# Kernel optimization log

Hardware: AMD Instinct MI355X
Metric: run time of the kernel (lower is better)

Reference implementation:

```python
import jax, jax.numpy as jnp
import numpy as np

N = 100000   # num nodes
E = 3200000  # num edges (avg degree 32)
EPS = 1e-5   # BatchNorm eps


def _gcn_norm(edge_index, edge_weight, n):
    # add self loops with weight 1 (PyG gcn_norm default fill_value=1.0)
    loops = jnp.arange(n, dtype=edge_index.dtype)
    ei = jnp.concatenate([edge_index, jnp.stack([loops, loops])], axis=1)
    ew = jnp.concatenate([edge_weight, jnp.ones((n,), edge_weight.dtype)])
    row, col = ei[0], ei[1]
    deg = jax.ops.segment_sum(ew, col, num_segments=n)
    deg_safe = jnp.where(deg > 0, deg, 1.0)
    dinv = jnp.where(deg > 0, jax.lax.rsqrt(deg_safe), 0.0)
    norm = dinv[row] * ew * dinv[col]  # [E+N]
    return row, col, norm


def _gcn_conv(x, row, col, norm, W, b, n):
    h = x @ W                                   # [N, out]
    msg = h[row] * norm[:, None]                # gather + scale, [E+N, out]
    out = jax.ops.segment_sum(msg, col, num_segments=n)  # scatter-add
    return out + b


def _bn(x, g, b, rm, rv):
    # BatchNorm1d in eval mode: running statistics
    return (x - rm) * jax.lax.rsqrt(rv + EPS) * g + b


def setup_inputs() -> dict:
    key = jax.random.key(0)
    ks = jax.random.split(key, 24)
    def p(i, shape, scale=1.0):
        return jax.random.normal(ks[i], shape, dtype=jnp.float32) * scale
    inp = {
        "x": p(0, (N, 1)),
        "edge_index": jax.random.randint(ks[1], (2, E), 0, N, dtype=jnp.int32),
        "edge_weight": jax.random.uniform(ks[2], (E,), dtype=jnp.float32),
        # GCNConv weights (glorot-ish scale) and biases
        "W1": p(3, (1, 16), 0.5), "b1": jnp.zeros((16,), jnp.float32),
        "W2": p(4, (16, 4), 0.25), "b2": jnp.zeros((4,), jnp.float32),
        "W3": p(5, (4, 1), 0.5), "b3": jnp.zeros((1,), jnp.float32),
        # BatchNorm params + running stats (running_var > 0)
        "g1": p(6, (16,), 0.1) + 1.0, "be1": p(7, (16,), 0.1),
        "rm1": p(8, (16,), 0.1), "rv1": jax.random.uniform(ks[9], (16,)) + 0.5,
        "g2": p(10, (4,), 0.1) + 1.0, "be2": p(11, (4,), 0.1),
        "rm2": p(12, (4,), 0.1), "rv2": jax.random.uniform(ks[13], (4,)) + 0.5,
        "g3": p(14, (1,), 0.1) + 1.0, "be3": p(15, (1,), 0.1),
        "rm3": p(16, (1,), 0.1), "rv3": jax.random.uniform(ks[17], (1,)) + 0.5,
        # end Linear(1, 1)
        "Wl": p(18, (1, 1)), "bl": p(19, (1,), 0.1),
    }
    return inp


def reference(x, edge_index, edge_weight,
              W1, b1, W2, b2, W3, b3,
              g1, be1, rm1, rv1,
              g2, be2, rm2, rv2,
              g3, be3, rm3, rv3,
              Wl, bl):
    row, col, norm = _gcn_norm(edge_index, edge_weight, N)
    h = _gcn_conv(x, row, col, norm, W1, b1, N)
    h = jax.nn.relu(_bn(h, g1, be1, rm1, rv1))  # dropout = identity in eval
    h = _gcn_conv(h, row, col, norm, W2, b2, N)
    h = jax.nn.relu(_bn(h, g2, be2, rm2, rv2))
    h = _gcn_conv(h, row, col, norm, W3, b3, N)
    h = _bn(h, g3, be3, rm3, rv3)
    h = h @ Wl + bl
    return jax.nn.sigmoid(h)
```

## Files before the change

### kernel.cpp

```cpp
#include <hip/hip_runtime.h>
#include <math.h>

#define NN 100000
#define NE 3200000
#define EPSBN 1e-5f

#define BSH 7
#define NB 782
#define NBLK 250
#define CHUNK 12800
#define C4 (CHUNK/4)
#define CAP 5120
#define BTA 512

#define NSB 12512
#define STCAP 4608

__global__ void k_params_zero(const float* __restrict__ W1, const float* __restrict__ b1,
                              const float* __restrict__ g1, const float* __restrict__ be1,
                              const float* __restrict__ rm1, const float* __restrict__ rv1,
                              const float* __restrict__ b2,
                              const float* __restrict__ g2, const float* __restrict__ be2,
                              const float* __restrict__ rm2, const float* __restrict__ rv2,
                              const float* __restrict__ b3,
                              const float* __restrict__ g3, const float* __restrict__ be3,
                              const float* __restrict__ rm3, const float* __restrict__ rv3,
                              const float* __restrict__ Wl, const float* __restrict__ bl,
                              float* __restrict__ P, int* __restrict__ cnt) {
    int f = threadIdx.x;
    for (int i = f; i < NB; i += 1024) cnt[i] = 0;
    if (f < 16) {
        float k = g1[f] * rsqrtf(rv1[f] + EPSBN);
        P[f]      = W1[f] * k;
        P[16 + f] = (b1[f] - rm1[f]) * k + be1[f];
    }
    if (f < 4) {
        float k = g2[f] * rsqrtf(rv2[f] + EPSBN);
        P[32 + f] = k;
        P[36 + f] = (b2[f] - rm2[f]) * k + be2[f];
    }
    if (f == 0) {
        float k = g3[0] * rsqrtf(rv3[0] + EPSBN);
        P[40] = k * Wl[0];
        P[41] = ((b3[0] - rm3[0]) * k + be3[0]) * Wl[0] + bl[0];
    }
}

__global__ void k_build(const int* __restrict__ row, const int* __restrict__ col,
                        const float* __restrict__ ew, int* __restrict__ cnt,
                        uint2* __restrict__ rec) {
    __shared__ int h[NB];
    __shared__ int base[NB];
    int blk = blockIdx.x, tid = threadIdx.x;
    for (int j = tid; j < NB; j += BTA) h[j] = 0;
    __syncthreads();
    const int4* c4 = (const int4*)(col + blk * CHUNK);
    int rk[7][4];
#pragma unroll
    for (int it = 0; it < 7; ++it) {
        int i = tid + it * BTA;
        if (i < C4) {
            int4 c = c4[i];
            rk[it][0] = atomicAdd(&h[c.x >> BSH], 1);
            rk[it][1] = atomicAdd(&h[c.y >> BSH], 1);
            rk[it][2] = atomicAdd(&h[c.z >> BSH], 1);
            rk[it][3] = atomicAdd(&h[c.w >> BSH], 1);
        }
    }
    __syncthreads();
    for (int j = tid; j < NB; j += BTA) {
        int hj = h[j];
        base[j] = hj ? atomicAdd(&cnt[j], hj) : 0;
    }
    __syncthreads();
    const int4*   r4 = (const int4*)(row + blk * CHUNK);
    const float4* w4 = (const float4*)(ew + blk * CHUNK);
#pragma unroll
    for (int it = 0; it < 7; ++it) {
        int i = tid + it * BTA;
        if (i < C4) {
            int4 c = c4[i]; int4 r = r4[i]; float4 w = w4[i];
            int b0 = c.x >> BSH, b1 = c.y >> BSH, b2 = c.z >> BSH, b3 = c.w >> BSH;
            rec[(size_t)b0 * CAP + base[b0] + rk[it][0]] =
                make_uint2((unsigned)r.x | ((unsigned)(c.x & 127) << 17), __float_as_uint(w.x));
            rec[(size_t)b1 * CAP + base[b1] + rk[it][1]] =
                make_uint2((unsigned)r.y | ((unsigned)(c.y & 127) << 17), __float_as_uint(w.y));
            rec[(size_t)b2 * CAP + base[b2] + rk[it][2]] =
                make_uint2((unsigned)r.z | ((unsigned)(c.z & 127) << 17), __float_as_uint(w.z));
            rec[(size_t)b3 * CAP + base[b3] + rk[it][3]] =
                make_uint2((unsigned)r.w | ((unsigned)(c.w & 127) << 17), __float_as_uint(w.w));
        }
    }
}

__global__ void k_subsort_deg(const int* __restrict__ cnt, uint2* __restrict__ rec,
                              int2* __restrict__ subsn, const float* __restrict__ x,
                              float* __restrict__ dinv, float* __restrict__ xd) {
    __shared__ uint2 st[STCAP];
    __shared__ int subtot[16];
    __shared__ int live[16];
    __shared__ int sstart[16];
    __shared__ int scount[16];
    int bin = blockIdx.x, tid = threadIdx.x;
    int lane = tid & 63, wv = tid >> 6;
    int n = cnt[bin];
    if (n > STCAP) n = STCAP;
    uint2* rb = rec + (size_t)bin * CAP;
    for (int i = tid; i < n; i += BTA) st[i] = rb[i];
    if (tid < 16) subtot[tid] = 0;
    __syncthreads();

    int myCnt = 0;
    for (int base = tid - lane; base < n; base += BTA) {
        int i = base + lane;
        bool v = (i < n);
        unsigned key = v ? ((st[i].x >> 20) & 15u) : 0u;
        unsigned long long bv = __ballot(v);
        unsigned long long b0 = __ballot(key & 1u);
        unsigned long long b1 = __ballot(key & 2u);
        unsigned long long b2 = __ballot(key & 4u);
        unsigned long long b3 = __ballot(key & 8u);
        if (lane < 16) {
            unsigned k = (unsigned)lane;
            unsigned long long m = bv;
            m &= (k & 1u) ? b0 : ~b0;
            m &= (k & 2u) ? b1 : ~b1;
            m &= (k & 4u) ? b2 : ~b2;
            m &= (k & 8u) ? b3 : ~b3;
            myCnt += __popcll(m);
        }
    }
    if (lane < 16 && myCnt) atomicAdd(&subtot[lane], myCnt);
    __syncthreads();

    if (tid == 0) {
        int run = 0;
        for (int k = 0; k < 16; ++k) {
            live[k] = run;
            sstart[k] = run;
            scount[k] = subtot[k];
            subsn[bin * 16 + k] = make_int2(bin * CAP + run, subtot[k]);
            run += subtot[k];
        }
    }
    __syncthreads();

    for (int base = tid - lane; base < n; base += BTA) {
        int i = base + lane;
        bool v = (i < n);
        uint2 rcd = v ? st[i] : make_uint2(0u, 0u);
        unsigned key = v ? ((rcd.x >> 20) & 15u) : 0u;
        unsigned long long bv = __ballot(v);
        unsigned long long b0 = __ballot(key & 1u);
        unsigned long long b1 = __ballot(key & 2u);
        unsigned long long b2 = __ballot(key & 4u);
        unsigned long long b3 = __ballot(key & 8u);
        int gb = 0;
        if (lane < 16) {
            unsigned k = (unsigned)lane;
            unsigned long long m = bv;
            m &= (k & 1u) ? b0 : ~b0;
            m &= (k & 2u) ? b1 : ~b1;
            m &= (k & 4u) ? b2 : ~b2;
            m &= (k & 8u) ? b3 : ~b3;
            int c = __popcll(m);
            if (c) gb = atomicAdd(&live[(int)k], c);
        }
        unsigned long long same = bv;
        same &= (key & 1u) ? b0 : ~b0;
        same &= (key & 2u) ? b1 : ~b1;
        same &= (key & 4u) ? b2 : ~b2;
        same &= (key & 8u) ? b3 : ~b3;
        unsigned long long below = (lane == 0) ? 0ull : ((~0ull) >> (64 - lane));
        int rank = __popcll(same & below);
        int mybase = __shfl(gb, (int)key);
        if (v) rb[mybase + rank] = rcd;
    }
    __syncthreads();

    for (int s = 0; s < 2; ++s) {
        int sb = (wv << 1) | s;
        int n0 = scount[sb];
        const uint2* p = rb + sstart[sb];
        float acc[8] = {0.f, 0.f, 0.f, 0.f, 0.f, 0.f, 0.f, 0.f};
        for (int i = lane; i < n0; i += 64) {
            uint2 v = p[i];
            int cl = (v.x >> 17) & 7;
            float w = __uint_as_float(v.y);
#pragma unroll
            for (int c = 0; c < 8; ++c) acc[c] += (cl == c) ? w : 0.f;
        }
#pragma unroll
        for (int c = 0; c < 8; ++c) {
            float a = acc[c];
            a += __shfl_xor(a, 1);  a += __shfl_xor(a, 2);  a += __shfl_xor(a, 4);
            a += __shfl_xor(a, 8);  a += __shfl_xor(a, 16); a += __shfl_xor(a, 32);
            acc[c] = a;
        }
        float mine = acc[0];
#pragma unroll
        for (int c = 1; c < 8; ++c) mine = (lane == c) ? acc[c] : mine;
        int colv = (bin << BSH) + (sb << 3) + lane;
        if (lane < 8 && colv < NN) {
            float d = rsqrtf(1.0f + mine);
            dinv[colv] = d;
            xd[colv] = x[colv] * d;
        }
    }
}


__global__ void k_agg1_2(const int2* __restrict__ subsn, const uint2* __restrict__ rec,
                         const float* __restrict__ dinv, const float* __restrict__ xd,
                         const float* __restrict__ P, const float* __restrict__ W2,
                         float* __restrict__ m2s) {
    __shared__ float sacc[8][8][32];
    int tid = threadIdx.x, lane = tid & 63, wv = tid >> 6;
    int b = blockIdx.x * 8 + wv;
    int2 sn = subsn[b];
    float acc[8] = {0.f, 0.f, 0.f, 0.f, 0.f, 0.f, 0.f, 0.f};
    for (int i = lane; i < sn.y; i += 64) {
        uint2 v = rec[sn.x + i];
        int cl = (v.x >> 17) & 7;
        float g = xd[v.x & 0x1FFFF] * __uint_as_float(v.y);
#pragma unroll
        for (int c = 0; c < 8; ++c) acc[c] += (cl == c) ? g : 0.f;
    }
#pragma unroll
    for (int c = 0; c < 8; ++c) acc[c] += __shfl_xor(acc[c], 32);
    if (lane < 32) {
#pragma unroll
        for (int c = 0; c < 8; ++c) sacc[wv][c][lane] = acc[c];
    }
    __syncthreads();
    if (tid < 64) {
        int w8 = tid >> 3, c = tid & 7;
        float s = 0.f;
        for (int l = 0; l < 32; ++l) s += sacc[w8][c][(l + tid) & 31];
        int colv = blockIdx.x * 64 + tid;
        if (colv < NN) {
            float dc = dinv[colv];
            float y = (s + xd[colv]) * dc;
            float m0 = 0.f, m1 = 0.f, m2v = 0.f, m3v = 0.f;
#pragma unroll
            for (int f = 0; f < 16; ++f) {
                float z = fmaxf(fmaf(y, P[f], P[16 + f]), 0.0f);
                m0 = fmaf(z, W2[f * 4 + 0], m0);
                m1 = fmaf(z, W2[f * 4 + 1], m1);
                m2v = fmaf(z, W2[f * 4 + 2], m2v);
                m3v = fmaf(z, W2[f * 4 + 3], m3v);
            }
            *(float4*)(m2s + 4 * colv) = make_float4(m0 * dc, m1 * dc, m2v * dc, m3v * dc);
        }
    }
}

__global__ void k_agg2_2(const int2* __restrict__ subsn, const uint2* __restrict__ rec,
                         const float* __restrict__ dinv, const float* __restrict__ m2s,
                         const float* __restrict__ P, const float* __restrict__ W3,
                         float* __restrict__ m3s) {
    __shared__ float sacc[8][8][4][32];
    __shared__ float sfin[8][8][4];
    int tid = threadIdx.x, lane = tid & 63, wv = tid >> 6;
    int b = blockIdx.x * 8 + wv;
    int2 sn = subsn[b];
    float acc[8][4];
#pragma unroll
    for (int c = 0; c < 8; ++c)
#pragma unroll
        for (int j = 0; j < 4; ++j) acc[c][j] = 0.f;
    for (int i = lane; i < sn.y; i += 64) {
        uint2 v = rec[sn.x + i];
        int cl = (v.x >> 17) & 7;
        float w = __uint_as_float(v.y);
        float4 m = *(const float4*)(m2s + 4 * (v.x & 0x1FFFF));
#pragma unroll
        for (int c = 0; c < 8; ++c) {
            float sel = (cl == c) ? w : 0.f;
            acc[c][0] = fmaf(m.x, sel, acc[c][0]);
            acc[c][1] = fmaf(m.y, sel, acc[c][1]);
            acc[c][2] = fmaf(m.z, sel, acc[c][2]);
            acc[c][3] = fmaf(m.w, sel, acc[c][3]);
        }
    }
#pragma unroll
    for (int c = 0; c < 8; ++c)
#pragma unroll
        for (int j = 0; j < 4; ++j) acc[c][j] += __shfl_xor(acc[c][j], 32);
    if (lane < 32) {
#pragma unroll
        for (int c = 0; c < 8; ++c)
#pragma unroll
            for (int j = 0; j < 4; ++j) sacc[wv][c][j][lane] = acc[c][j];
    }
    __syncthreads();
    if (tid < 256) {
        int w8 = tid >> 5, c = (tid >> 2) & 7, j = tid & 3;
        float s = 0.f;
        for (int l = 0; l < 32; ++l) s += sacc[w8][c][j][(l + tid) & 31];
        sfin[w8][c][j] = s;
    }
    __syncthreads();
    if (tid < 64) {
        int w8 = tid >> 3, c = tid & 7;
        int colv = blockIdx.x * 64 + tid;
        if (colv < NN) {
            float dc = dinv[colv];
            float4 mc = *(const float4*)(m2s + 4 * colv);
            float a0 = (sfin[w8][c][0] + mc.x) * dc;
            float a1 = (sfin[w8][c][1] + mc.y) * dc;
            float a2 = (sfin[w8][c][2] + mc.z) * dc;
            float a3 = (sfin[w8][c][3] + mc.w) * dc;
            float v3 = 0.f;
            v3 = fmaf(fmaxf(fmaf(a0, P[32], P[36]), 0.f), W3[0], v3);
            v3 = fmaf(fmaxf(fmaf(a1, P[33], P[37]), 0.f), W3[1], v3);
            v3 = fmaf(fmaxf(fmaf(a2, P[34], P[38]), 0.f), W3[2], v3);
            v3 = fmaf(fmaxf(fmaf(a3, P[35], P[39]), 0.f), W3[3], v3);
            m3s[colv] = v3 * dc;
        }
    }
}

__global__ void k_agg3_2(const int2* __restrict__ subsn, const uint2* __restrict__ rec,
                         const float* __restrict__ dinv, const float* __restrict__ m3s,
                         const float* __restrict__ P, float* __restrict__ out) {
    __shared__ float sacc[8][8][32];
    int tid = threadIdx.x, lane = tid & 63, wv = tid >> 6;
    int b = blockIdx.x * 8 + wv;
    int2 sn = subsn[b];
    float acc[8] = {0.f, 0.f, 0.f, 0.f, 0.f, 0.f, 0.f, 0.f};
    for (int i = lane; i < sn.y; i += 64) {
        uint2 v = rec[sn.x + i];
        int cl = (v.x >> 17) & 7;
        float g = m3s[v.x & 0x1FFFF] * __uint_as_float(v.y);
#pragma unroll
        for (int c = 0; c < 8; ++c) acc[c] += (cl == c) ? g : 0.f;
    }
#pragma unroll
    for (int c = 0; c < 8; ++c) acc[c] += __shfl_xor(acc[c], 32);
    if (lane < 32) {
#pragma unroll
        for (int c = 0; c < 8; ++c) sacc[wv][c][lane] = acc[c];
    }
    __syncthreads();
    if (tid < 64) {
        int w8 = tid >> 3, c = tid & 7;
        float s = 0.f;
        for (int l = 0; l < 32; ++l) s += sacc[w8][c][(l + tid) & 31];
        int colv = blockIdx.x * 64 + tid;
        if (colv < NN) {
            float t = fmaf((s + m3s[colv]) * dinv[colv], P[40], P[41]);
            out[colv] = 1.0f / (1.0f + __expf(-t));
        }
    }
}


__global__ void k_init_deg(float* __restrict__ deg) {
    int i = blockIdx.x * blockDim.x + threadIdx.x;
    if (i < NN) deg[i] = 1.0f;
}

__global__ void k_dinv_y1(const float* __restrict__ deg, const float* __restrict__ x,
                          float* __restrict__ dinv, float* __restrict__ y1) {
    int i = blockIdx.x * blockDim.x + threadIdx.x;
    if (i >= NN) return;
    float d = rsqrtf(deg[i]);
    dinv[i] = d;
    y1[i] = x[i] * d * d;
}

__global__ void k_l1_epi(const float* __restrict__ y1, const float* __restrict__ dinv,
                         const float* __restrict__ P, const float* __restrict__ W2,
                         float* __restrict__ m2, float* __restrict__ agg2) {
    int i = blockIdx.x * blockDim.x + threadIdx.x;
    if (i >= NN) return;
    float y = y1[i];
    float m0 = 0.f, m1 = 0.f, m2v = 0.f, m3v = 0.f;
#pragma unroll
    for (int f = 0; f < 16; ++f) {
        float z = fmaxf(fmaf(y, P[f], P[16 + f]), 0.0f);
        m0 = fmaf(z, W2[f * 4 + 0], m0);
        m1 = fmaf(z, W2[f * 4 + 1], m1);
        m2v = fmaf(z, W2[f * 4 + 2], m2v);
        m3v = fmaf(z, W2[f * 4 + 3], m3v);
    }
    float d = dinv[i];
    float d2 = d * d;
    *(float4*)(m2 + 4 * i)   = make_float4(m0, m1, m2v, m3v);
    *(float4*)(agg2 + 4 * i) = make_float4(m0 * d2, m1 * d2, m2v * d2, m3v * d2);
}

__global__ void k_l2_epi(const float* __restrict__ agg2, const float* __restrict__ dinv,
                         const float* __restrict__ P, const float* __restrict__ W3,
                         float* __restrict__ m3, float* __restrict__ agg3) {
    int i = blockIdx.x * blockDim.x + threadIdx.x;
    if (i >= NN) return;
    float4 a = *(const float4*)(agg2 + 4 * i);
    float v = 0.f;
    v = fmaf(fmaxf(fmaf(a.x, P[32], P[36]), 0.f), W3[0], v);
    v = fmaf(fmaxf(fmaf(a.y, P[33], P[37]), 0.f), W3[1], v);
    v = fmaf(fmaxf(fmaf(a.z, P[34], P[38]), 0.f), W3[2], v);
    v = fmaf(fmaxf(fmaf(a.w, P[35], P[39]), 0.f), W3[3], v);
    float d = dinv[i];
    m3[i] = v;
    agg3[i] = v * d * d;
}

__global__ void k_final(const float* __restrict__ agg3, const float* __restrict__ P,
                        float* __restrict__ out) {
    int i = blockIdx.x * blockDim.x + threadIdx.x;
    if (i >= NN) return;
    float t = fmaf(agg3[i], P[40], P[41]);
    out[i] = 1.0f / (1.0f + __expf(-t));
}

__global__ void k_deg(const int* __restrict__ col, const float* __restrict__ ew,
                      float* __restrict__ deg) {
    int e = (blockIdx.x * blockDim.x + threadIdx.x) * 4;
    if (e >= NE) return;
    int4 c = *(const int4*)(col + e);
    float4 w = *(const float4*)(ew + e);
    atomicAdd(&deg[c.x], w.x);
    atomicAdd(&deg[c.y], w.y);
    atomicAdd(&deg[c.z], w.z);
    atomicAdd(&deg[c.w], w.w);
}

__global__ void k_norm_agg1(const int* __restrict__ row, const int* __restrict__ col,
                            const float* __restrict__ ew, const float* __restrict__ dinv,
                            const float* __restrict__ x,
                            float* __restrict__ norm, float* __restrict__ y1) {
    int e = (blockIdx.x * blockDim.x + threadIdx.x) * 4;
    if (e >= NE) return;
    int4 r = *(const int4*)(row + e);
    int4 c = *(const int4*)(col + e);
    float4 w = *(const float4*)(ew + e);
    float4 nv;
    nv.x = dinv[r.x] * w.x * dinv[c.x];
    nv.y = dinv[r.y] * w.y * dinv[c.y];
    nv.z = dinv[r.z] * w.z * dinv[c.z];
    nv.w = dinv[r.w] * w.w * dinv[c.w];
    *(float4*)(norm + e) = nv;
    atomicAdd(&y1[c.x], x[r.x] * nv.x);
    atomicAdd(&y1[c.y], x[r.y] * nv.y);
    atomicAdd(&y1[c.z], x[r.z] * nv.z);
    atomicAdd(&y1[c.w], x[r.w] * nv.w);
}

__global__ void k_agg2(const int* __restrict__ row, const int* __restrict__ col,
                       const float* __restrict__ norm, const float* __restrict__ m2,
                       float* __restrict__ agg2) {
    int e = blockIdx.x * blockDim.x + threadIdx.x;
    if (e >= NE) return;
    int r = row[e], c = col[e];
    float nv = norm[e];
    float4 m = *(const float4*)(m2 + 4 * r);
    atomicAdd(&agg2[4 * c + 0], m.x * nv);
    atomicAdd(&agg2[4 * c + 1], m.y * nv);
    atomicAdd(&agg2[4 * c + 2], m.z * nv);
    atomicAdd(&agg2[4 * c + 3], m.w * nv);
}

__global__ void k_agg3(const int* __restrict__ row, const int* __restrict__ col,
                       const float* __restrict__ norm, const float* __restrict__ m3,
                       float* __restrict__ agg3) {
    int e = (blockIdx.x * blockDim.x + threadIdx.x) * 4;
    if (e >= NE) return;
    int4 r = *(const int4*)(row + e);
    int4 c = *(const int4*)(col + e);
    float4 nv = *(const float4*)(norm + e);
    atomicAdd(&agg3[c.x], m3[r.x] * nv.x);
    atomicAdd(&agg3[c.y], m3[r.y] * nv.y);
    atomicAdd(&agg3[c.z], m3[r.z] * nv.z);
    atomicAdd(&agg3[c.w], m3[r.w] * nv.w);
}


extern "C" void kernel_launch(void* const* d_in, const int* in_sizes, int n_in,
                              void* d_out, int out_size, void* d_ws, size_t ws_size,
                              hipStream_t stream) {
    const float* x  = (const float*)d_in[0];
    const int*   ei = (const int*)d_in[1];
    const float* ew = (const float*)d_in[2];
    const float* W1 = (const float*)d_in[3];
    const float* b1 = (const float*)d_in[4];
    const float* W2 = (const float*)d_in[5];
    const float* b2 = (const float*)d_in[6];
    const float* W3 = (const float*)d_in[7];
    const float* b3 = (const float*)d_in[8];
    const float* g1 = (const float*)d_in[9];
    const float* be1 = (const float*)d_in[10];
    const float* rm1 = (const float*)d_in[11];
    const float* rv1 = (const float*)d_in[12];
    const float* g2 = (const float*)d_in[13];
    const float* be2 = (const float*)d_in[14];
    const float* rm2 = (const float*)d_in[15];
    const float* rv2 = (const float*)d_in[16];
    const float* g3 = (const float*)d_in[17];
    const float* be3 = (const float*)d_in[18];
    const float* rm3 = (const float*)d_in[19];
    const float* rv3 = (const float*)d_in[20];
    const float* Wl = (const float*)d_in[21];
    const float* bl = (const float*)d_in[22];
    float* out = (float*)d_out;

    const int* row = ei;
    const int* col = ei + NE;

    const int BT = 256;
    const int gN = (NN + BT - 1) / BT;
    const int gE4 = (NE / 4 + BT - 1) / BT;

    char* ws = (char*)d_ws;

    if (ws_size >= 37000000u) {
        float* P     = (float*)(ws);
        int*   cnt   = (int*)  (ws + 4096);
        int2*  subsn = (int2*) (ws + 16384);
        float* dinv  = (float*)(ws + 524288);
        float* xd    = (float*)(ws + 1048576);
        float* m3s   = (float*)(ws + 1572864);
        float* m2s   = (float*)(ws + 2097152);
        uint2* rec   = (uint2*)(ws + 4194304);

        k_params_zero<<<1, 1024, 0, stream>>>(W1, b1, g1, be1, rm1, rv1,
                                              b2, g2, be2, rm2, rv2,
                                              b3, g3, be3, rm3, rv3, Wl, bl, P, cnt);
        k_build<<<NBLK, BTA, 0, stream>>>(row, col, ew, cnt, rec);
        k_subsort_deg<<<NB, BTA, 0, stream>>>(cnt, rec, subsn, x, dinv, xd);
        k_agg1_2<<<NSB / 8, BTA, 0, stream>>>(subsn, rec, dinv, xd, P, W2, m2s);
        k_agg2_2<<<NSB / 8, BTA, 0, stream>>>(subsn, rec, dinv, m2s, P, W3, m3s);
        k_agg3_2<<<NSB / 8, BTA, 0, stream>>>(subsn, rec, dinv, m3s, P, out);
    } else {
        float* deg   = (float*)(ws);
        float* dinv  = (float*)(ws + 400000);
        float* y1    = (float*)(ws + 800000);
        float* m2    = (float*)(ws + 1200000);
        float* agg2  = (float*)(ws + 2800000);
        float* m3    = (float*)(ws + 4400000);
        float* agg3  = (float*)(ws + 4800000);
        float* Pf    = (float*)(ws + 5200000);
        float* norm  = (float*)(ws + 5200256);
        const int gE1 = (NE + BT - 1) / BT;

        k_params_zero<<<1, 1024, 0, stream>>>(W1, b1, g1, be1, rm1, rv1,
                                              b2, g2, be2, rm2, rv2,
                                              b3, g3, be3, rm3, rv3, Wl, bl, Pf, (int*)(ws + 5300000));
        k_init_deg<<<gN, BT, 0, stream>>>(deg);
        k_deg<<<gE4, BT, 0, stream>>>(col, ew, deg);
        k_dinv_y1<<<gN, BT, 0, stream>>>(deg, x, dinv, y1);
        k_norm_agg1<<<gE4, BT, 0, stream>>>(row, col, ew, dinv, x, norm, y1);
        k_l1_epi<<<gN, BT, 0, stream>>>(y1, dinv, Pf, W2, m2, agg2);
        k_agg2<<<(NE + BT - 1) / BT, BT, 0, stream>>>(row, col, norm, m2, agg2);
        k_l2_epi<<<gN, BT, 0, stream>>>(agg2, dinv, Pf, W3, m3, agg3);
        k_agg3<<<gE4, BT, 0, stream>>>(row, col, norm, m3, agg3);
        k_final<<<gN, BT, 0, stream>>>(agg3, Pf, out);
    }
}
```

Baseline: 135.3 us.

## Stage bucketed edge records in shared memory for coalesced global scatter

The build kernel now computes a local exclusive prefix over the per-block bin histogram and first scatters edge records into a shared-memory buffer sorted by bin. It then writes them to global memory in sorted order, so consecutive threads write contiguous runs within each bin instead of scattered 8-byte stores. Chunk size is halved and the block count doubled so the staging buffer fits in LDS. The cost is extra shared memory (about 64KB per block), which lowers occupancy, plus a serial 98-step scan on one thread.

```diff
diff --git a/kernel.cpp b/kernel.cpp
--- a/kernel.cpp
+++ b/kernel.cpp
@@ -7,8 +7,8 @@
 
 #define BSH 7
 #define NB 782
-#define NBLK 250
-#define CHUNK 12800
+#define NBLK 500
+#define CHUNK 6400
 #define C4 (CHUNK/4)
 #define CAP 5120
 #define BTA 512
@@ -50,14 +50,18 @@
                         const float* __restrict__ ew, int* __restrict__ cnt,
                         uint2* __restrict__ rec) {
     __shared__ int h[NB];
-    __shared__ int base[NB];
+    __shared__ int gb[NB];
+    __shared__ int gsum[98];
+    __shared__ uint2 st[CHUNK];
+    __shared__ unsigned short sb[CHUNK];
     int blk = blockIdx.x, tid = threadIdx.x;
     for (int j = tid; j < NB; j += BTA) h[j] = 0;
     __syncthreads();
+
     const int4* c4 = (const int4*)(col + blk * CHUNK);
-    int rk[7][4];
-#pragma unroll
-    for (int it = 0; it < 7; ++it) {
+    int rk[4][4];
+#pragma unroll
+    for (int it = 0; it < 4; ++it) {
         int i = tid + it * BTA;
         if (i < C4) {
             int4 c = c4[i];
@@ -68,28 +72,61 @@
         }
     }
     __syncthreads();
+
     for (int j = tid; j < NB; j += BTA) {
         int hj = h[j];
-        base[j] = hj ? atomicAdd(&cnt[j], hj) : 0;
-    }
-    __syncthreads();
+        gb[j] = hj ? atomicAdd(&cnt[j], hj) : 0;
+    }
+
+    if (tid < 98) {
+        int s = 0, b0 = tid * 8;
+#pragma unroll
+        for (int k = 0; k < 8; ++k) { int idx = b0 + k; s += (idx < NB) ? h[idx] : 0; }
+        gsum[tid] = s;
+    }
+    __syncthreads();
+    if (tid == 0) {
+        int run = 0;
+        for (int g = 0; g < 98; ++g) { int t = gsum[g]; gsum[g] = run; run += t; }
+    }
+    __syncthreads();
+    if (tid < 98) {
+        int run = gsum[tid], b0 = tid * 8;
+#pragma unroll
+        for (int k = 0; k < 8; ++k) {
+            int idx = b0 + k;
+            if (idx < NB) { int t = h[idx]; h[idx] = run; run += t; }
+        }
+    }
+    __syncthreads();
+
     const int4*   r4 = (const int4*)(row + blk * CHUNK);
     const float4* w4 = (const float4*)(ew + blk * CHUNK);
 #pragma unroll
-    for (int it = 0; it < 7; ++it) {
+    for (int it = 0; it < 4; ++it) {
         int i = tid + it * BTA;
         if (i < C4) {
             int4 c = c4[i]; int4 r = r4[i]; float4 w = w4[i];
             int b0 = c.x >> BSH, b1 = c.y >> BSH, b2 = c.z >> BSH, b3 = c.w >> BSH;
-            rec[(size_t)b0 * CAP + base[b0] + rk[it][0]] =
-                make_uint2((unsigned)r.x | ((unsigned)(c.x & 127) << 17), __float_as_uint(w.x));
-            rec[(size_t)b1 * CAP + base[b1] + rk[it][1]] =
-                make_uint2((unsigned)r.y | ((unsigned)(c.y & 127) << 17), __float_as_uint(w.y));
-            rec[(size_t)b2 * CAP + base[b2] + rk[it][2]] =
-                make_uint2((unsigned)r.z | ((unsigned)(c.z & 127) << 17), __float_as_uint(w.z));
-            rec[(size_t)b3 * CAP + base[b3] + rk[it][3]] =
-                make_uint2((unsigned)r.w | ((unsigned)(c.w & 127) << 17), __float_as_uint(w.w));
-        }
+            int s0 = h[b0] + rk[it][0];
+            st[s0] = make_uint2((unsigned)r.x | ((unsigned)(c.x & 127) << 17), __float_as_uint(w.x));
+            sb[s0] = (unsigned short)b0;
+            int s1 = h[b1] + rk[it][1];
+            st[s1] = make_uint2((unsigned)r.y | ((unsigned)(c.y & 127) << 17), __float_as_uint(w.y));
+            sb[s1] = (unsigned short)b1;
+            int s2 = h[b2] + rk[it][2];
+            st[s2] = make_uint2((unsigned)r.z | ((unsigned)(c.z & 127) << 17), __float_as_uint(w.z));
+            sb[s2] = (unsigned short)b2;
+            int s3 = h[b3] + rk[it][3];
+            st[s3] = make_uint2((unsigned)r.w | ((unsigned)(c.w & 127) << 17), __float_as_uint(w.w));
+            sb[s3] = (unsigned short)b3;
+        }
+    }
+    __syncthreads();
+
+    for (int i = tid; i < CHUNK; i += BTA) {
+        int b = sb[i];
+        rec[(size_t)b * CAP + gb[b] + (i - h[b])] = st[i];
     }
 }
 
```

After: 121.7 us. 10.1% less time.
